# Performance work log

Hardware: AMD Instinct MI355X
Metric: run time of the kernel (lower is better)

## Reference

```python
import jax, jax.numpy as jnp
import numpy as np

S, B, C, H, M = 384, 8, 1024, 16, 1536
CC = C // H


def setup_inputs() -> dict:
    key = jax.random.key(0)
    ks = jax.random.split(key, 8)
    x = jax.random.normal(ks[0], (S, B, C), dtype=jnp.float32)
    pe = jax.random.normal(ks[1], (S, B, C), dtype=jnp.float32)
    memory_k = jax.random.normal(ks[2], (M, B, H, CC), dtype=jnp.float32)
    memory_v = jax.random.normal(ks[3], (M, B, H, CC), dtype=jnp.float32)
    w_qkv = jax.random.normal(ks[4], (C, 3 * C), dtype=jnp.float32) * 0.02
    b_qkv = jnp.zeros((3 * C,), dtype=jnp.float32)
    w_out = jax.random.normal(ks[5], (C, C), dtype=jnp.float32) * 0.02
    b_out = jnp.zeros((C,), dtype=jnp.float32)
    terminal = jnp.zeros((B,), dtype=bool)
    # causal mask over the new tokens: True = masked (future positions)
    content_mask = jnp.broadcast_to(
        (jnp.arange(S)[None, :] > jnp.arange(S)[:, None])[:, :, None], (S, S, B))
    padding_mask = jnp.zeros((S, B), dtype=bool)  # True = padded
    memory_length = jax.random.randint(ks[6], (B,), 0, M, dtype=jnp.int32)
    return dict(x=x, positional_encoding=pe, memory_k=memory_k, memory_v=memory_v,
                w_qkv=w_qkv, b_qkv=b_qkv, w_out=w_out, b_out=b_out,
                terminal=terminal, content_mask=content_mask,
                padding_mask=padding_mask, memory_length=memory_length)


def reference(x, positional_encoding, memory_k, memory_v, w_qkv, b_qkv,
              w_out, b_out, terminal, content_mask, padding_mask, memory_length):
    s, b, c = x.shape
    # qkv projection
    qkv = (x + positional_encoding) @ w_qkv + b_qkv          # [s,b,3c]
    q, k, v = jnp.split(qkv, 3, axis=-1)
    q = q.reshape(s, b, H, CC)
    k = k.reshape(s, b, H, CC)
    v = v.reshape(s, b, H, CC)
    # clear_memory(terminal): zero lengths for terminal episodes
    mem_len = jnp.where(terminal, 0, memory_length)          # [b]
    # ragged memory concat expressed with fixed capacity M + padding mask
    k_full = jnp.concatenate([memory_k, k], axis=0)          # [M+s,b,H,CC]
    v_full = jnp.concatenate([memory_v, v], axis=0)
    mem_pad = jnp.arange(M)[:, None] >= mem_len[None, :]     # [M,b] True=masked
    kv_pad = jnp.concatenate([mem_pad, padding_mask], axis=0)  # [M+s,b]
    mem_content = jnp.zeros((s, M, b), dtype=bool)           # memory visible to all queries
    full_content = jnp.concatenate([mem_content, content_mask], axis=1)  # [s,M+s,b]
    mask = full_content | kv_pad[None, :, :]                 # [s,M+s,b]
    # attention
    scores = jnp.einsum('sbhc,tbhc->stbh', q, k_full) * (1.0 / np.sqrt(CC))
    scores = jnp.where(mask[:, :, :, None], jnp.float32(-1e9), scores)
    p = jax.nn.softmax(scores, axis=1)                       # [s,M+s,b,h]
    out = jnp.einsum('stbh,tbhc->sbhc', p, v_full).reshape(s, b, c)
    return out @ w_out + b_out
```

## Files before the change

### kernel.cpp

```cpp
#include <hip/hip_runtime.h>
#include <math.h>

#define S_DIM 384
#define B_DIM 8
#define C_DIM 1024
#define H_DIM 16
#define M_DIM 1536
#define CC_DIM 64
#define ROWS  (S_DIM * B_DIM)
#define N3C   (3 * C_DIM)
#define CHUNK 6
#define MAXS  5

typedef unsigned short u16;
typedef short bf8v  __attribute__((ext_vector_type(8)));
typedef short bf4v  __attribute__((ext_vector_type(4)));
typedef u16   us8   __attribute__((ext_vector_type(8)));
typedef u16   us4   __attribute__((ext_vector_type(4)));
typedef float f4v   __attribute__((ext_vector_type(4)));

__device__ __forceinline__ u16 f2bf(float f) {
    unsigned u = __float_as_uint(f);
    u += 0x7fffu + ((u >> 16) & 1u);
    return (u16)(u >> 16);
}
__device__ __forceinline__ float bf2f(u16 v) {
    return __uint_as_float(((unsigned)v) << 16);
}
#if __has_builtin(__builtin_amdgcn_exp2f)
#define EX2(x) __builtin_amdgcn_exp2f(x)
#else
#define EX2(x) __expf((x) * 0.69314718056f)
#endif
#define QSCALE (0.125f * 1.44269504f)

__device__ __forceinline__ f4v mfma16x16x16bf16(bf4v a, bf4v b, f4v c) {
#if __has_builtin(__builtin_amdgcn_mfma_f32_16x16x16bf16_1k)
    return __builtin_amdgcn_mfma_f32_16x16x16bf16_1k(a, b, c, 0, 0, 0);
#else
    return c;
#endif
}

__device__ __forceinline__ void gload16(const u16* g, u16* l) {
    __builtin_amdgcn_global_load_lds(
        (const __attribute__((address_space(1))) void*)g,
        (__attribute__((address_space(3))) void*)l, 16, 0, 0);
}

__device__ __forceinline__ void tr_direct8(const float* __restrict__ in,
                                           u16* __restrict__ out,
                                           int R, int Cc, int r0, int c0, int tid) {
    const int c4 = c0 + (tid & 15) * 4;
    const int rq = r0 + (tid >> 4) * 8;
    float4 L[8];
    #pragma unroll
    for (int k = 0; k < 8; k++)
        L[k] = *(const float4*)(in + (size_t)(rq + k) * Cc + c4);
    #pragma unroll
    for (int j = 0; j < 4; j++) {
        us8 o;
        #pragma unroll
        for (int k = 0; k < 8; k++)
            o[k] = f2bf(((const float*)&L[k])[j]);
        *(us8*)(out + (size_t)(c4 + j) * R + rq) = o;
    }
}

__global__ __launch_bounds__(256) void prep_all(
    const float* __restrict__ x, const float* __restrict__ pe, u16* __restrict__ Abf,
    const float* __restrict__ wqkv, u16* __restrict__ Wqkvt,
    const float* __restrict__ wout, u16* __restrict__ Woutt,
    const float* __restrict__ mk, u16* __restrict__ mk_bf,
    const float* __restrict__ mv, u16* __restrict__ mv_t,
    const unsigned char* __restrict__ terminal, const int* __restrict__ mem_len)
{
    const int bid = blockIdx.x, tid = threadIdx.x;

    if (bid < 1536) {
        const int bh = bid & 127, tg = bid >> 7;
        const int t0 = tg * 128;
        const int b = bh >> 4;
        const int L = terminal[b] ? 0 : mem_len[b];
        const int Lc = ((L + 63) >> 6) << 6;
        if (t0 >= Lc) return;
        const int cc4 = (tid & 15) * 4;
        const int tq = t0 + (tid >> 4) * 8;
        float4 Lv[8];
        #pragma unroll
        for (int k = 0; k < 8; k++)
            Lv[k] = *(const float4*)(mv + ((size_t)(tq + k) * 128 + bh) * 64 + cc4);
        #pragma unroll
        for (int j = 0; j < 4; j++) {
            us8 o;
            #pragma unroll
            for (int k = 0; k < 8; k++)
                o[k] = f2bf(((const float*)&Lv[k])[j]);
            *(us8*)(mv_t + ((size_t)bh * 64 + cc4 + j) * M_DIM + tq) = o;
        }
    } else if (bid < 4608) {
        const int b6 = bid - 1536;
        const int b = b6 & 7, t0 = (b6 >> 3) * 4;
        const int L = terminal[b] ? 0 : mem_len[b];
        const int Lc = ((L + 63) >> 6) << 6;
        if (t0 >= Lc) return;
        const int r = t0 + (tid >> 6);
        const size_t rb = (size_t)r * 8192 + (size_t)b * 1024;
        const int cw = (tid & 63) * 4;
        float4 v[4];
        #pragma unroll
        for (int j = 0; j < 4; j++)
            v[j] = *(const float4*)(mk + rb + cw + j * 256);
        #pragma unroll
        for (int j = 0; j < 4; j++) {
            us4 o;
            o[0] = f2bf(v[j].x); o[1] = f2bf(v[j].y);
            o[2] = f2bf(v[j].z); o[3] = f2bf(v[j].w);
            *(us4*)(mk_bf + rb + cw + j * 256) = o;
        }
    } else if (bid < 5376) {
        size_t i0 = (size_t)(bid - 4608) * 4096 + tid * 16;
        float4 xv[4], pv[4];
        #pragma unroll
        for (int j = 0; j < 4; j++) {
            xv[j] = *(const float4*)(x + i0 + j * 4);
            pv[j] = *(const float4*)(pe + i0 + j * 4);
        }
        #pragma unroll
        for (int h8 = 0; h8 < 2; h8++) {
            us8 o;
            #pragma unroll
            for (int j = 0; j < 2; j++) {
                float4 a = xv[h8 * 2 + j], p = pv[h8 * 2 + j];
                o[j * 4 + 0] = f2bf(a.x + p.x);
                o[j * 4 + 1] = f2bf(a.y + p.y);
                o[j * 4 + 2] = f2bf(a.z + p.z);
                o[j * 4 + 3] = f2bf(a.w + p.w);
            }
            *(us8*)(Abf + i0 + h8 * 8) = o;
        }
    } else if (bid < 5760) {
        const int b2 = bid - 5376;
        tr_direct8(wqkv, Wqkvt, C_DIM, N3C, (b2 / 48) * 128, (b2 % 48) * 64, tid);
    } else {
        const int b3 = bid - 5760;
        tr_direct8(wout, Woutt, C_DIM, C_DIM, (b3 / 16) * 128, (b3 % 16) * 64, tid);
    }
}

__global__ __launch_bounds__(256) void qkv_gemm(
    const u16* __restrict__ Abf, const u16* __restrict__ Wt,
    const float* __restrict__ bias,
    u16* __restrict__ Qw, u16* __restrict__ Kw, u16* __restrict__ Vwt)
{
    __shared__ u16 smem[128 * 64 + 64 * 64];
    u16* As = smem;
    u16* Bs = smem + 128 * 64;
    u16* Cs = smem;

    const int tid = threadIdx.x;
    const int lane = tid & 63, w = tid >> 6;
    const int lr = lane & 15, quad = lane >> 4;
    const int wm = w >> 1, wn = w & 1;
    const int row0 = blockIdx.y * 128, col0 = blockIdx.x * 64;

    f4v acc[4][2];
    #pragma unroll
    for (int i = 0; i < 4; i++)
        #pragma unroll
        for (int j = 0; j < 2; j++)
            acc[i][j] = (f4v){0.f, 0.f, 0.f, 0.f};

    for (int k0 = 0; k0 < C_DIM; k0 += 64) {
        __syncthreads();
        #pragma unroll
        for (int j = 0; j < 4; j++) {
            int idx = j * 256 + tid;
            int r = idx >> 3, c = (idx & 7) ^ (r & 7);
            gload16(&Abf[(size_t)(row0 + r) * C_DIM + k0 + c * 8], &As[idx * 8]);
        }
        #pragma unroll
        for (int j = 0; j < 2; j++) {
            int idx = j * 256 + tid;
            int r = idx >> 3, c = (idx & 7) ^ (r & 7);
            gload16(&Wt[(size_t)(col0 + r) * C_DIM + k0 + c * 8], &Bs[idx * 8]);
        }
        __syncthreads();
        #pragma unroll
        for (int kh = 0; kh < 2; kh++) {
            bf8v a[4], b[2];
            #pragma unroll
            for (int mi = 0; mi < 4; mi++) {
                int row = wm * 64 + mi * 16 + lr;
                int p = (kh * 4 + quad) ^ (lr & 7);
                a[mi] = *(const bf8v*)&As[row * 64 + p * 8];
            }
            #pragma unroll
            for (int nj = 0; nj < 2; nj++) {
                int row = wn * 32 + nj * 16 + lr;
                int p = (kh * 4 + quad) ^ (lr & 7);
                b[nj] = *(const bf8v*)&Bs[row * 64 + p * 8];
            }
            #pragma unroll
            for (int mi = 0; mi < 4; mi++)
                #pragma unroll
                for (int nj = 0; nj < 2; nj++)
                    acc[mi][nj] = __builtin_amdgcn_mfma_f32_16x16x32_bf16(a[mi], b[nj], acc[mi][nj], 0, 0, 0);
        }
    }

    const int which = col0 >> 10;
    const int h = (col0 >> 6) & 15;
    const float qs = (which == 0) ? QSCALE : 1.0f;

    __syncthreads();
    #pragma unroll
    for (int nj = 0; nj < 2; nj++) {
        int col = col0 + wn * 32 + nj * 16 + lr;
        float bv = bias[col];
        #pragma unroll
        for (int mi = 0; mi < 4; mi++)
            #pragma unroll
            for (int reg = 0; reg < 4; reg++)
                Cs[(wm * 64 + mi * 16 + quad * 4 + reg) * 72 + wn * 32 + nj * 16 + lr] =
                    f2bf((acc[mi][nj][reg] + bv) * qs);
    }
    __syncthreads();

    if (which != 2) {
        u16* dstbuf = (which == 0) ? Qw : Kw;
        int r = tid >> 1, half = tid & 1;
        int rg = row0 + r, s = rg >> 3, bb = rg & 7;
        u16* drow = dstbuf + ((size_t)(bb * 16 + h) * S_DIM + s) * 64 + half * 32;
        #pragma unroll
        for (int i = 0; i < 4; i++)
            *(us8*)(drow + i * 8) = *(const us8*)&Cs[r * 72 + half * 32 + i * 8];
    } else {
        int cc = tid & 63, w4 = tid >> 6;
        int s0 = row0 >> 3;
        #pragma unroll
        for (int pb = 0; pb < 2; pb++) {
            int bb = w4 * 2 + pb;
            us8 v0, v1;
            #pragma unroll
            for (int sl = 0; sl < 8; sl++) {
                v0[sl] = Cs[(sl * 8 + bb) * 72 + cc];
                v1[sl] = Cs[((sl + 8) * 8 + bb) * 72 + cc];
            }
            u16* dr = Vwt + ((size_t)(bb * 16 + h) * 64 + cc) * S_DIM + s0;
            *(us8*)dr = v0;
            *(us8*)(dr + 8) = v1;
        }
    }
}

__global__ __launch_bounds__(256) void attn_split(
    const u16* __restrict__ Qw, const u16* __restrict__ Kw,
    const u16* __restrict__ mk_bf, const u16* __restrict__ Vwt,
    const u16* __restrict__ mv_t, const unsigned char* __restrict__ terminal,
    const int* __restrict__ mem_len, u16* __restrict__ Op, float* __restrict__ ml)
{
    __shared__ u16 Ks[64 * 64];
    __shared__ u16 Vs[64 * 64];

    const int tid = threadIdx.x;
    const int lane = tid & 63, w = tid >> 6;
    const int lr = lane & 15, quad = lane >> 4, q8 = quad * 8;
    const int bid = blockIdx.x;
    const int j = bid % MAXS;
    const int g = bid / MAXS;
    const int b = g & 7, h = (g >> 3) & 15, sc = g >> 7;
    const int bh = b * 16 + h, sq0 = sc * 64;
    const int L = terminal[b] ? 0 : mem_len[b];
    const int memChunks = (L + 63) >> 6;
    const int total = memChunks + sc + 1;
    const int lo = j * CHUNK;
    const int hi = (lo + CHUNK < total) ? lo + CHUNK : total;
    if (lo >= total) return;

    const int qrow = sq0 + w * 16 + lr;

    const u16* qbase = Qw + ((size_t)bh * S_DIM + sq0 + w * 16 + lr) * 64;
    bf8v qf0 = *(const bf8v*)&qbase[q8];
    bf8v qf1 = *(const bf8v*)&qbase[32 + q8];

    f4v O[4];
    #pragma unroll
    for (int nj = 0; nj < 4; nj++) O[nj] = (f4v){0.f, 0.f, 0.f, 0.f};
    float m_i = -1e30f, l_i = 0.0f;

    const f4v zero = (f4v){0.f, 0.f, 0.f, 0.f};

    for (int ch = lo; ch < hi; ch++) {
        const bool isMem = (ch < memChunks);
        const int tloc = isMem ? ch * 64 : (ch - memChunks) * 64;
        const u16* kb; size_t kstr;
        if (isMem) { kb = mk_bf + ((size_t)tloc * 128 + bh) * 64; kstr = 128 * 64; }
        else       { kb = Kw + ((size_t)bh * S_DIM + tloc) * 64; kstr = 64; }
        const u16* vb; size_t vstr;
        if (isMem) { vb = mv_t + (size_t)bh * 64 * M_DIM + tloc; vstr = M_DIM; }
        else       { vb = Vwt + (size_t)bh * 64 * S_DIM + tloc; vstr = S_DIM; }

        __syncthreads();
        #pragma unroll
        for (int jj = 0; jj < 2; jj++) {
            int idx = jj * 256 + tid;
            int r = idx >> 3, c = (idx & 7) ^ (r & 7);
            gload16(kb + (size_t)r * kstr + c * 8, &Ks[idx * 8]);
        }
        #pragma unroll
        for (int jj = 0; jj < 2; jj++) {
            int idx = jj * 256 + tid;
            int cc = idx >> 3, c = (idx & 7) ^ (cc & 7);
            gload16(vb + (size_t)cc * vstr + c * 8, &Vs[idx * 8]);
        }
        __syncthreads();

        f4v sv[4];
        __builtin_amdgcn_s_setprio(1);
        #pragma unroll
        for (int tt = 0; tt < 4; tt++) {
            int row = tt * 16 + lr;
            int p0 = quad ^ (lr & 7), p1 = (4 + quad) ^ (lr & 7);
            bf8v k0 = *(const bf8v*)&Ks[row * 64 + p0 * 8];
            bf8v k1 = *(const bf8v*)&Ks[row * 64 + p1 * 8];
            sv[tt] = __builtin_amdgcn_mfma_f32_16x16x32_bf16(k0, qf0, zero, 0, 0, 0);
            sv[tt] = __builtin_amdgcn_mfma_f32_16x16x32_bf16(k1, qf1, sv[tt], 0, 0, 0);
        }
        __builtin_amdgcn_s_setprio(0);

        if (isMem) {
            if (tloc + 64 > L) {
                #pragma unroll
                for (int tt = 0; tt < 4; tt++)
                    #pragma unroll
                    for (int reg = 0; reg < 4; reg++) {
                        int t = tloc + tt * 16 + quad * 4 + reg;
                        if (t >= L) sv[tt][reg] = -1e30f;
                    }
            }
        } else {
            if (tloc + 63 > sq0 + w * 16) {
                #pragma unroll
                for (int tt = 0; tt < 4; tt++)
                    #pragma unroll
                    for (int reg = 0; reg < 4; reg++) {
                        int t = tloc + tt * 16 + quad * 4 + reg;
                        if (t > qrow) sv[tt][reg] = -1e30f;
                    }
            }
        }

        float rowmax = fmaxf(fmaxf(sv[0][0], sv[0][1]), fmaxf(sv[0][2], sv[0][3]));
        #pragma unroll
        for (int tt = 1; tt < 4; tt++)
            rowmax = fmaxf(rowmax, fmaxf(fmaxf(sv[tt][0], sv[tt][1]),
                                         fmaxf(sv[tt][2], sv[tt][3])));
        rowmax = fmaxf(rowmax, __shfl_xor(rowmax, 16));
        rowmax = fmaxf(rowmax, __shfl_xor(rowmax, 32));
        float mnew = fmaxf(m_i, rowmax);
        float alpha = EX2(m_i - mnew);
        m_i = mnew;
        float sum = 0.0f;
        bf4v pf[4];
        #pragma unroll
        for (int tt = 0; tt < 4; tt++) {
            #pragma unroll
            for (int reg = 0; reg < 4; reg++) {
                float p = EX2(sv[tt][reg] - mnew);
                sum += p;
                pf[tt][reg] = (short)f2bf(p);
            }
        }
        sum += __shfl_xor(sum, 16);
        sum += __shfl_xor(sum, 32);
        l_i = l_i * alpha + sum;

        float alphaR[4];
        #pragma unroll
        for (int reg = 0; reg < 4; reg++)
            alphaR[reg] = __shfl(alpha, quad * 4 + reg);
        #pragma unroll
        for (int nj = 0; nj < 4; nj++)
            #pragma unroll
            for (int reg = 0; reg < 4; reg++)
                O[nj][reg] *= alphaR[reg];

        __builtin_amdgcn_s_setprio(1);
        #pragma unroll
        for (int tt = 0; tt < 4; tt++) {
            #pragma unroll
            for (int nj = 0; nj < 4; nj++) {
                int cc = nj * 16 + lr;
                int c = (tt * 2 + (quad >> 1)) ^ (lr & 7);
                bf4v vf = *(const bf4v*)&Vs[cc * 64 + c * 8 + (quad & 1) * 4];
                O[nj] = mfma16x16x16bf16(pf[tt], vf, O[nj]);
            }
        }
        __builtin_amdgcn_s_setprio(0);
    }

    const size_t pbase = (size_t)(g * MAXS + j) * 64;
    if (quad == 0) {
        int row = w * 16 + lr;
        float2 mlv = {m_i, l_i};
        *(float2*)&ml[(pbase + row) * 2] = mlv;
    }
    #pragma unroll
    for (int reg = 0; reg < 4; reg++) {
        int row = w * 16 + quad * 4 + reg;
        #pragma unroll
        for (int nj = 0; nj < 4; nj++)
            Op[(pbase + row) * 64 + nj * 16 + lr] = f2bf(O[nj][reg]);
    }
}

__global__ __launch_bounds__(256) void attn_combine(
    const unsigned char* __restrict__ terminal, const int* __restrict__ mem_len,
    const u16* __restrict__ Op, const float* __restrict__ ml, u16* __restrict__ Obf)
{
    const int g = blockIdx.x;
    const int b = g & 7, h = (g >> 3) & 15, sc = g >> 7;
    const int tid = threadIdx.x;
    const int row = tid >> 2, c0 = (tid & 3) * 16;

    const int L = terminal[b] ? 0 : mem_len[b];
    const int total = ((L + 63) >> 6) + sc + 1;
    const int nsp = (total + CHUNK - 1) / CHUNK;

    float m[MAXS], lv[MAXS];
    #pragma unroll
    for (int j = 0; j < MAXS; j++) {
        if (j < nsp) {
            size_t base = (size_t)(g * MAXS + j) * 64 + row;
            m[j]  = ml[base * 2];
            lv[j] = ml[base * 2 + 1];
        } else { m[j] = -1e30f; lv[j] = 0.0f; }
    }
    float mstar = m[0];
    #pragma unroll
    for (int j = 1; j < MAXS; j++) mstar = fmaxf(mstar, m[j]);
    float sc_j[MAXS], l = 0.0f;
    #pragma unroll
    for (int j = 0; j < MAXS; j++) {
        sc_j[j] = (j < nsp) ? EX2(m[j] - mstar) : 0.0f;
        l += sc_j[j] * lv[j];
    }
    float inv = 1.0f / l;

    float o[16];
    #pragma unroll
    for (int c = 0; c < 16; c++) o[c] = 0.0f;
    for (int j = 0; j < nsp; j++) {
        const u16* src = &Op[((size_t)(g * MAXS + j) * 64 + row) * 64 + c0];
        us8 v0 = *(const us8*)src;
        us8 v1 = *(const us8*)(src + 8);
        #pragma unroll
        for (int c = 0; c < 8; c++) {
            o[c]     += sc_j[j] * bf2f(v0[c]);
            o[c + 8] += sc_j[j] * bf2f(v1[c]);
        }
    }
    int s = sc * 64 + row;
    size_t dst = ((size_t)s * 8 + b) * C_DIM + h * 64 + c0;
    us8 w0, w1;
    #pragma unroll
    for (int c = 0; c < 8; c++) {
        w0[c] = f2bf(o[c] * inv);
        w1[c] = f2bf(o[c + 8] * inv);
    }
    *(us8*)&Obf[dst] = w0;
    *(us8*)&Obf[dst + 8] = w1;
}

__global__ __launch_bounds__(256) void proj_gemm(
    const u16* __restrict__ Abf, const u16* __restrict__ Wt,
    const float* __restrict__ bias, float* __restrict__ out)
{
    __shared__ u16 As[64 * 64];
    __shared__ u16 Bs[64 * 64];
    const int tid = threadIdx.x;
    const int lane = tid & 63, w = tid >> 6;
    const int lr = lane & 15, quad = lane >> 4;
    const int row0 = blockIdx.y * 64, col0 = blockIdx.x * 64;

    f4v acc[4];
    #pragma unroll
    for (int i = 0; i < 4; i++) acc[i] = (f4v){0.f, 0.f, 0.f, 0.f};

    for (int k0 = 0; k0 < C_DIM; k0 += 64) {
        __syncthreads();
        #pragma unroll
        for (int j = 0; j < 2; j++) {
            int idx = j * 256 + tid;
            int r = idx >> 3, c = (idx & 7) ^ (r & 7);
            gload16(&Abf[(size_t)(row0 + r) * C_DIM + k0 + c * 8], &As[idx * 8]);
            gload16(&Wt[(size_t)(col0 + r) * C_DIM + k0 + c * 8], &Bs[idx * 8]);
        }
        __syncthreads();
        #pragma unroll
        for (int kh = 0; kh < 2; kh++) {
            int p = (kh * 4 + quad) ^ (lr & 7);
            bf8v a = *(const bf8v*)&As[(w * 16 + lr) * 64 + p * 8];
            #pragma unroll
            for (int nj = 0; nj < 4; nj++) {
                bf8v bfr = *(const bf8v*)&Bs[(nj * 16 + lr) * 64 + p * 8];
                acc[nj] = __builtin_amdgcn_mfma_f32_16x16x32_bf16(a, bfr, acc[nj], 0, 0, 0);
            }
        }
    }

    #pragma unroll
    for (int nj = 0; nj < 4; nj++) {
        int col = col0 + nj * 16 + lr;
        float bv = bias[col];
        #pragma unroll
        for (int reg = 0; reg < 4; reg++) {
            int rg = row0 + w * 16 + quad * 4 + reg;
            out[(size_t)rg * C_DIM + col] = acc[nj][reg] + bv;
        }
    }
}

extern "C" void kernel_launch(void* const* d_in, const int* in_sizes, int n_in,
                              void* d_out, int out_size, void* d_ws, size_t ws_size,
                              hipStream_t stream) {
    const float* x    = (const float*)d_in[0];
    const float* pe   = (const float*)d_in[1];
    const float* mk   = (const float*)d_in[2];
    const float* mv   = (const float*)d_in[3];
    const float* wqkv = (const float*)d_in[4];
    const float* bqkv = (const float*)d_in[5];
    const float* wout = (const float*)d_in[6];
    const float* bout = (const float*)d_in[7];
    const unsigned char* term = (const unsigned char*)d_in[8];
    const int* mem_len = (const int*)d_in[11];

    char* ws = (char*)d_ws;
    u16* Abf   = (u16*)(ws + 0);
    u16* Obf   = (u16*)(ws + 0);
    u16* Wqkvt = (u16*)(ws + 6291456);
    float* ml  = (float*)(ws + 6291456);
    u16* Woutt = (u16*)(ws + 12582912);
    u16* mk_bf = (u16*)(ws + 14680064);
    u16* mv_t  = (u16*)(ws + 39845888);
    u16* Qw    = (u16*)(ws + 65011712);
    u16* Kw    = (u16*)(ws + 71303168);
    u16* Vwt   = (u16*)(ws + 77594624);
    u16* Op    = (u16*)(ws + 83886080);

    float* out = (float*)d_out;

    prep_all<<<5888, 256, 0, stream>>>(x, pe, Abf, wqkv, Wqkvt, wout, Woutt,
                                       mk, mk_bf, mv, mv_t, term, mem_len);

    qkv_gemm<<<dim3(N3C / 64, ROWS / 128), 256, 0, stream>>>(
        Abf, Wqkvt, bqkv, Qw, Kw, Vwt);

    attn_split<<<B_DIM * H_DIM * (S_DIM / 64) * MAXS, 256, 0, stream>>>(
        Qw, Kw, mk_bf, Vwt, mv_t, term, mem_len, Op, ml);

    attn_combine<<<B_DIM * H_DIM * (S_DIM / 64), 256, 0, stream>>>(
        term, mem_len, Op, ml, Obf);

    proj_gemm<<<dim3(C_DIM / 64, ROWS / 64), 256, 0, stream>>>(
        Obf, Woutt, bout, out);
}
```

Before: 274.9 us.

## Double-buffer K/V tiles in split attention to overlap loads with MFMA

Splits the shared K/V tiles into two buffers and issues the next chunk's global-to-LDS loads before computing on the current chunk. Explicit vmcnt waits and raw barriers replace the two __syncthreads per iteration, so memory latency is meant to hide behind the QK and PV MFMA work. This doubles LDS use to 32KB per block, which may lower occupancy, and each block handles at most 6 chunks, so there is little steady state to pipeline.

```diff
diff --git a/kernel.cpp b/kernel.cpp
--- a/kernel.cpp
+++ b/kernel.cpp
@@ -260,8 +260,8 @@
     const u16* __restrict__ mv_t, const unsigned char* __restrict__ terminal,
     const int* __restrict__ mem_len, u16* __restrict__ Op, float* __restrict__ ml)
 {
-    __shared__ u16 Ks[64 * 64];
-    __shared__ u16 Vs[64 * 64];
+    __shared__ u16 KsAll[2][64 * 64];
+    __shared__ u16 VsAll[2][64 * 64];
 
     const int tid = threadIdx.x;
     const int lane = tid & 63, w = tid >> 6;
@@ -291,7 +291,7 @@
 
     const f4v zero = (f4v){0.f, 0.f, 0.f, 0.f};
 
-    for (int ch = lo; ch < hi; ch++) {
+    auto stagef = [&](int ch, int buf) {
         const bool isMem = (ch < memChunks);
         const int tloc = isMem ? ch * 64 : (ch - memChunks) * 64;
         const u16* kb; size_t kstr;
@@ -300,21 +300,38 @@
         const u16* vb; size_t vstr;
         if (isMem) { vb = mv_t + (size_t)bh * 64 * M_DIM + tloc; vstr = M_DIM; }
         else       { vb = Vwt + (size_t)bh * 64 * S_DIM + tloc; vstr = S_DIM; }
-
-        __syncthreads();
         #pragma unroll
         for (int jj = 0; jj < 2; jj++) {
             int idx = jj * 256 + tid;
             int r = idx >> 3, c = (idx & 7) ^ (r & 7);
-            gload16(kb + (size_t)r * kstr + c * 8, &Ks[idx * 8]);
+            gload16(kb + (size_t)r * kstr + c * 8, &KsAll[buf][idx * 8]);
         }
         #pragma unroll
         for (int jj = 0; jj < 2; jj++) {
             int idx = jj * 256 + tid;
             int cc = idx >> 3, c = (idx & 7) ^ (cc & 7);
-            gload16(vb + (size_t)cc * vstr + c * 8, &Vs[idx * 8]);
-        }
-        __syncthreads();
+            gload16(vb + (size_t)cc * vstr + c * 8, &VsAll[buf][idx * 8]);
+        }
+    };
+
+    int cur = 0;
+    stagef(lo, 0);
+
+    for (int ch = lo; ch < hi; ch++) {
+        if (ch + 1 < hi) {
+            stagef(ch + 1, cur ^ 1);
+            asm volatile("s_waitcnt vmcnt(4)" ::: "memory");
+        } else {
+            asm volatile("s_waitcnt vmcnt(0)" ::: "memory");
+        }
+        __builtin_amdgcn_sched_barrier(0);
+        __builtin_amdgcn_s_barrier();
+        __builtin_amdgcn_sched_barrier(0);
+
+        const u16* Ks = &KsAll[cur][0];
+        const u16* Vs = &VsAll[cur][0];
+        const bool isMem = (ch < memChunks);
+        const int tloc = isMem ? ch * 64 : (ch - memChunks) * 64;
 
         f4v sv[4];
         __builtin_amdgcn_s_setprio(1);
@@ -398,6 +415,10 @@
             }
         }
         __builtin_amdgcn_s_setprio(0);
+
+        __builtin_amdgcn_sched_barrier(0);
+        __builtin_amdgcn_s_barrier();
+        cur ^= 1;
     }
 
     const size_t pbase = (size_t)(g * MAXS + j) * 64;
```

Measured after the change: 282.6 us. 1.03x slower.
